# Kernel tuning notes

Hardware: AMD Instinct MI355X
Metric: run time of the kernel (lower is better)

Reference implementation:

```python
import jax, jax.numpy as jnp
import numpy as np

D_MODEL = 1024
NHEAD = 16
HEAD_DIM = D_MODEL // NHEAD
B, T = 2, 2048


def setup_inputs() -> dict:
    key = jax.random.key(0)
    ks = jax.random.split(key, 11)
    s = 1.0 / np.sqrt(D_MODEL)
    inp = {
        'q': jax.random.normal(ks[0], (B, T, D_MODEL), jnp.float32),
        'k': jax.random.normal(ks[1], (B, T, D_MODEL), jnp.float32),
        'v': jax.random.normal(ks[2], (B, T, D_MODEL), jnp.float32),
        'Wq': jax.random.normal(ks[3], (D_MODEL, D_MODEL), jnp.float32) * s,
        'bq': jnp.zeros((D_MODEL,), jnp.float32),
        'Wk': jax.random.normal(ks[4], (D_MODEL, D_MODEL), jnp.float32) * s,
        'bk': jnp.zeros((D_MODEL,), jnp.float32),
        'Wv': jax.random.normal(ks[5], (D_MODEL, D_MODEL), jnp.float32) * s,
        'bv': jnp.zeros((D_MODEL,), jnp.float32),
        'Wo': jax.random.normal(ks[6], (D_MODEL, D_MODEL), jnp.float32) * s,
        'bo': jnp.zeros((D_MODEL,), jnp.float32),
    }
    return inp


def reference(q, k, v, Wq, bq, Wk, bk, Wv, bv, Wo, bo):
    scale = np.sqrt(HEAD_DIM).astype(np.float32)
    # projections (torch Linear: x @ W.T + b), split heads -> [B, H, T, Dh]
    def proj(x, W, b):
        y = jnp.einsum('btd,ed->bte', x, W) + b
        return y.reshape(B, T, NHEAD, HEAD_DIM).transpose(0, 2, 1, 3)
    qh = proj(q, Wq, bq)
    kh = proj(k, Wk, bk)
    vh = proj(v, Wv, bv)
    scores = jnp.einsum('bhqd,bhkd->bhqk', qh, kh) / scale  # [B,H,T,T]
    weights = jax.nn.softmax(scores, axis=-1)
    out = jnp.einsum('bhqk,bhkd->bhqd', weights, vh)        # [B,H,T,Dh]
    out = out.transpose(0, 2, 1, 3).reshape(B, T, D_MODEL)
    return jnp.einsum('btd,ed->bte', out, Wo) + bo
```

## Files before the change

kernel.cpp:

```cpp
#include <hip/hip_runtime.h>
#include <cstdint>
#include <cstddef>


#define D_MODEL 1024
#define NHEAD   16
#define HDIM    64
#define BATCH   2
#define SEQ     2048
#define BT      (BATCH * SEQ)

typedef __bf16 bf16;
typedef __bf16 bf16x8 __attribute__((ext_vector_type(8)));
typedef __bf16 bf16x4 __attribute__((ext_vector_type(4)));
typedef float  floatx4 __attribute__((ext_vector_type(4)));
typedef short  short4v __attribute__((ext_vector_type(4)));

#define MFMA16(a, b, c) __builtin_amdgcn_mfma_f32_16x16x32_bf16((a), (b), (c), 0, 0, 0)

__device__ __forceinline__ floatx4 MFMA16B(bf16x4 a, bf16x4 b, floatx4 c) {
  return __builtin_amdgcn_mfma_f32_16x16x16bf16_1k(
      __builtin_bit_cast(short4v, a), __builtin_bit_cast(short4v, b), c, 0, 0, 0);
}

__device__ __forceinline__ void async_cp16(const bf16* g, bf16* l) {
  __builtin_amdgcn_global_load_lds(
      (__attribute__((address_space(1))) void*)(g),
      (__attribute__((address_space(3))) void*)(l), 16, 0, 0);
}

__global__ __launch_bounds__(256) void cvt7(
    const float* __restrict__ s0, const float* __restrict__ s1,
    const float* __restrict__ s2, const float* __restrict__ s3,
    const float* __restrict__ s4, const float* __restrict__ s5,
    const float* __restrict__ s6,
    bf16* __restrict__ d0, bf16* __restrict__ d1, bf16* __restrict__ d2,
    bf16* __restrict__ d3, bf16* __restrict__ d4, bf16* __restrict__ d5,
    bf16* __restrict__ d6)
{
  const float* src; bf16* dst; int n4;
  switch (blockIdx.y) {
    case 0:  src = s0; dst = d0; n4 = (BT * D_MODEL) / 4; break;
    case 1:  src = s1; dst = d1; n4 = (BT * D_MODEL) / 4; break;
    case 2:  src = s2; dst = d2; n4 = (BT * D_MODEL) / 4; break;
    case 3:  src = s3; dst = d3; n4 = (D_MODEL * D_MODEL) / 4; break;
    case 4:  src = s4; dst = d4; n4 = (D_MODEL * D_MODEL) / 4; break;
    case 5:  src = s5; dst = d5; n4 = (D_MODEL * D_MODEL) / 4; break;
    default: src = s6; dst = d6; n4 = (D_MODEL * D_MODEL) / 4; break;
  }
  int stride = gridDim.x * blockDim.x;
  for (int i = blockIdx.x * blockDim.x + threadIdx.x; i < n4; i += stride) {
    float4 f = ((const float4*)src)[i];
    bf16x4 h;
    h[0] = (bf16)f.x; h[1] = (bf16)f.y; h[2] = (bf16)f.z; h[3] = (bf16)f.w;
    ((bf16x4*)dst)[i] = h;
  }
}

__device__ __forceinline__ void gemm128_core(
    const bf16* __restrict__ A, const bf16* __restrict__ W,
    int m0, int n0, bf16* As, bf16* Bs, floatx4 acc[4][4])
{
  const int t = threadIdx.x;
  const int l = t & 63, w = t >> 6;
  const int quad = l >> 4, lr = l & 15;
  const int wm = (w >> 1) * 64, wn = (w & 1) * 64;

  floatx4 z = {0.f, 0.f, 0.f, 0.f};
#pragma unroll
  for (int i = 0; i < 4; i++)
#pragma unroll
    for (int j = 0; j < 4; j++) acc[i][j] = z;

  for (int kt = 0; kt < 1024; kt += 32) {
    __syncthreads();
#pragma unroll
    for (int i = 0; i < 2; i++) {
      int c = i * 256 + t;
      int row = c >> 2, ci = c & 3;
      async_cp16(A + (size_t)(m0 + row) * 1024 + kt + ci * 8,
                 As + (i * 256 + w * 64) * 8);
      async_cp16(W + (size_t)(n0 + row) * 1024 + kt + ci * 8,
                 Bs + (i * 256 + w * 64) * 8);
    }
    __syncthreads();

    bf16x8 af[4], bfr[4];
#pragma unroll
    for (int i = 0; i < 4; i++) {
      af[i]  = *(const bf16x8*)(As + (wm + i * 16 + lr) * 32 + quad * 8);
      bfr[i] = *(const bf16x8*)(Bs + (wn + i * 16 + lr) * 32 + quad * 8);
    }
#pragma unroll
    for (int i = 0; i < 4; i++)
#pragma unroll
      for (int j = 0; j < 4; j++)
        acc[i][j] = MFMA16(af[i], bfr[j], acc[i][j]);
  }
}

__global__ __launch_bounds__(256) void qkv_gemm(
    const bf16* __restrict__ qb, const bf16* __restrict__ kb, const bf16* __restrict__ vb,
    const bf16* __restrict__ wq, const bf16* __restrict__ wk, const bf16* __restrict__ wv,
    const float* __restrict__ biasq, const float* __restrict__ biask, const float* __restrict__ biasv,
    bf16* __restrict__ qh, bf16* __restrict__ kh, bf16* __restrict__ vt)
{
  __shared__ bf16 As[128 * 32];
  __shared__ bf16 Bs[128 * 32];
  const int zid = blockIdx.z;
  const bf16* A = (zid == 0) ? qb : ((zid == 1) ? kb : vb);
  const bf16* W = (zid == 0) ? wq : ((zid == 1) ? wk : wv);
  const float* bias = (zid == 0) ? biasq : ((zid == 1) ? biask : biasv);
  const int m0 = blockIdx.x * 128, n0 = blockIdx.y * 128;

  floatx4 acc[4][4];
  gemm128_core(A, W, m0, n0, As, Bs, acc);

  const int t = threadIdx.x, l = t & 63, w = t >> 6;
  const int quad = l >> 4, lr = l & 15;
  const int wm = (w >> 1) * 64, wn = (w & 1) * 64;

  if (zid < 2) {
    bf16* out = (zid == 0) ? qh : kh;
#pragma unroll
    for (int i = 0; i < 4; i++) {
      int mbase = m0 + wm + i * 16 + quad * 4;
      int b  = mbase >> 11;
      int tq = mbase & 2047;
#pragma unroll
      for (int j = 0; j < 4; j++) {
        int n = n0 + wn + j * 16 + lr;
        float bv = bias[n];
        int h = n >> 6, dh = n & 63;
        bf16* p = out + ((size_t)((b * NHEAD + h) * SEQ + tq)) * HDIM + dh;
#pragma unroll
        for (int r = 0; r < 4; r++)
          p[(size_t)r * HDIM] = (bf16)(acc[i][j][r] + bv);
      }
    }
  } else {
#pragma unroll
    for (int i = 0; i < 4; i++) {
      int mbase = m0 + wm + i * 16 + quad * 4;
      int b  = mbase >> 11;
      int tq = mbase & 2047;
#pragma unroll
      for (int j = 0; j < 4; j++) {
        int n = n0 + wn + j * 16 + lr;
        float bv = bias[n];
        int h = n >> 6, dh = n & 63;
        bf16x4 pk;
#pragma unroll
        for (int r = 0; r < 4; r++) pk[r] = (bf16)(acc[i][j][r] + bv);
        *(bf16x4*)(vt + ((size_t)((b * NHEAD + h) * HDIM + dh)) * SEQ + tq) = pk;
      }
    }
  }
}

__global__ __launch_bounds__(512, 4) void attn_fused(
    const bf16* __restrict__ qh, const bf16* __restrict__ kh,
    const bf16* __restrict__ vt, bf16* __restrict__ attn)
{
  __shared__ __align__(16) char smem[35840];
  bf16* Ks  = (bf16*)smem;
  bf16* Vts = (bf16*)(smem + 18432);
  bf16* Ost = (bf16*)smem;

  const int t = threadIdx.x, l = t & 63, w = t >> 6;
  const int quad = l >> 4, lr = l & 15;
  const int bh = blockIdx.y;
  const int qt0 = blockIdx.x * 128;
  const bf16* qg = qh + (size_t)bh * SEQ * HDIM;
  const bf16* kg = kh + (size_t)bh * SEQ * HDIM;
  const bf16* vg = vt + (size_t)bh * HDIM * SEQ;

  bf16x8 qf[2];
#pragma unroll
  for (int ko = 0; ko < 2; ko++)
    qf[ko] = *(const bf16x8*)(qg + (size_t)(qt0 + w * 16 + lr) * HDIM
                              + ko * 32 + quad * 8);

  floatx4 zz = {0.f, 0.f, 0.f, 0.f};
  floatx4 Oacc[4];
#pragma unroll
  for (int dt = 0; dt < 4; dt++) Oacc[dt] = zz;
  float mrow = -3.0e38f, lrow = 0.f;
  const float scale = 0.125f;

  for (int kt0 = 0; kt0 < SEQ; kt0 += 128) {
    __syncthreads();
#pragma unroll
    for (int i = 0; i < 2; i++) {
      int c = t + 512 * i;
      { int row = c >> 3, ci = c & 7;
        *(int4*)(Ks + row * 72 + ci * 8) =
            *(const int4*)(kg + (size_t)(kt0 + row) * HDIM + ci * 8); }
      { int row = c >> 4, ci = c & 15;
        *(int4*)(Vts + row * 136 + ci * 8) =
            *(const int4*)(vg + (size_t)row * SEQ + kt0 + ci * 8); }
    }
    __syncthreads();

    floatx4 s[8];
#pragma unroll
    for (int ni = 0; ni < 8; ni++) {
      const bf16* krow = Ks + (ni * 16 + lr) * 72 + quad * 8;
      bf16x8 k0 = *(const bf16x8*)(krow);
      bf16x8 k1 = *(const bf16x8*)(krow + 32);
      floatx4 a = zz;
      a = MFMA16(k0, qf[0], a);
      a = MFMA16(k1, qf[1], a);
      s[ni] = a;
    }

    float rmax = s[0][0];
#pragma unroll
    for (int ni = 0; ni < 8; ni++)
#pragma unroll
      for (int r = 0; r < 4; r++) rmax = fmaxf(rmax, s[ni][r]);
    rmax = fmaxf(rmax, __shfl_xor(rmax, 16, 64));
    rmax = fmaxf(rmax, __shfl_xor(rmax, 32, 64));
    float mnew = fmaxf(mrow, rmax * scale);
    float al = __expf(mrow - mnew);
    mrow = mnew;

    bf16x4 pk[8];
    float rsum = 0.f;
#pragma unroll
    for (int ni = 0; ni < 8; ni++)
#pragma unroll
      for (int r = 0; r < 4; r++) {
        float pv = __expf(s[ni][r] * scale - mnew);
        rsum += pv;
        pk[ni][r] = (bf16)pv;
      }
    rsum += __shfl_xor(rsum, 16, 64);
    rsum += __shfl_xor(rsum, 32, 64);
    lrow = lrow * al + rsum;
#pragma unroll
    for (int dt = 0; dt < 4; dt++)
#pragma unroll
      for (int r = 0; r < 4; r++) Oacc[dt][r] *= al;

#pragma unroll
    for (int ni = 0; ni < 8; ni++)
#pragma unroll
      for (int dt = 0; dt < 4; dt++) {
        bf16x4 vf = *(const bf16x4*)(Vts + (dt * 16 + lr) * 136
                                     + ni * 16 + quad * 4);
        Oacc[dt] = MFMA16B(vf, pk[ni], Oacc[dt]);
      }
  }

  float inv = 1.0f / lrow;
  __syncthreads();
#pragma unroll
  for (int dt = 0; dt < 4; dt++) {
    bf16x4 ov;
#pragma unroll
    for (int r = 0; r < 4; r++) ov[r] = (bf16)(Oacc[dt][r] * inv);
    *(bf16x4*)(Ost + (size_t)(w * 16 + lr) * 72 + dt * 16 + quad * 4) = ov;
  }
  __syncthreads();

  const int b = bh >> 4, h = bh & 15;
#pragma unroll
  for (int i = 0; i < 2; i++) {
    int c = t + 512 * i;
    int row = c >> 3, ci = c & 7;
    *(int4*)(attn + ((size_t)b * SEQ + qt0 + row) * D_MODEL + h * HDIM + ci * 8) =
        *(const int4*)(Ost + row * 72 + ci * 8);
  }
}

__global__ __launch_bounds__(256) void oproj_gemm(
    const bf16* __restrict__ attn, const bf16* __restrict__ wo,
    const float* __restrict__ bo, float* __restrict__ out)
{
  __shared__ bf16 As[128 * 32];
  __shared__ bf16 Bs[128 * 32];
  const int m0 = blockIdx.x * 128, n0 = blockIdx.y * 128;

  floatx4 acc[4][4];
  gemm128_core(attn, wo, m0, n0, As, Bs, acc);

  const int t = threadIdx.x, l = t & 63, w = t >> 6;
  const int quad = l >> 4, lr = l & 15;
  const int wm = (w >> 1) * 64, wn = (w & 1) * 64;

#pragma unroll
  for (int i = 0; i < 4; i++) {
    int m = m0 + wm + i * 16 + quad * 4;
#pragma unroll
    for (int j = 0; j < 4; j++) {
      int n = n0 + wn + j * 16 + lr;
      float bv = bo[n];
      float* p = out + (size_t)m * D_MODEL + n;
#pragma unroll
      for (int r = 0; r < 4; r++)
        p[(size_t)r * D_MODEL] = acc[i][j][r] + bv;
    }
  }
}

extern "C" void kernel_launch(void* const* d_in, const int* in_sizes, int n_in,
                              void* d_out, int out_size, void* d_ws, size_t ws_size,
                              hipStream_t stream)
{
  const float* q  = (const float*)d_in[0];
  const float* k  = (const float*)d_in[1];
  const float* v  = (const float*)d_in[2];
  const float* Wq = (const float*)d_in[3];
  const float* bq = (const float*)d_in[4];
  const float* Wk = (const float*)d_in[5];
  const float* bk = (const float*)d_in[6];
  const float* Wv = (const float*)d_in[7];
  const float* bv = (const float*)d_in[8];
  const float* Wo = (const float*)d_in[9];
  const float* bo = (const float*)d_in[10];

  const size_t NQ = (size_t)BT * D_MODEL;
  const size_t NW = (size_t)D_MODEL * D_MODEL;

  bf16* p = (bf16*)d_ws;
  bf16* qb   = p; p += NQ;
  bf16* kb   = p; p += NQ;
  bf16* vb   = p; p += NQ;
  bf16* wqb  = p; p += NW;
  bf16* wkb  = p; p += NW;
  bf16* wvb  = p; p += NW;
  bf16* wob  = p; p += NW;
  bf16* qhp  = p; p += NQ;
  bf16* khp  = p; p += NQ;
  bf16* vtp  = p; p += NQ;
  bf16* attn = p; p += NQ;

  cvt7<<<dim3(1024, 7, 1), 256, 0, stream>>>(q, k, v, Wq, Wk, Wv, Wo,
                                             qb, kb, vb, wqb, wkb, wvb, wob);
  qkv_gemm<<<dim3(32, 8, 3), 256, 0, stream>>>(qb, kb, vb, wqb, wkb, wvb,
                                               bq, bk, bv, qhp, khp, vtp);
  attn_fused<<<dim3(16, 32, 1), 512, 0, stream>>>(qhp, khp, vtp, attn);
  oproj_gemm<<<dim3(32, 8, 1), 256, 0, stream>>>(attn, wob, bo, (float*)d_out);
}
```

Measured before the change: 238.6 us.

## Split attention keys across wave halves, fold scale into Q, shrink oproj tiles

Folds the softmax scale and log2(e) into the Q projection so the attention softmax can use exp2 directly. The attention kernel now handles 64 query rows per block, with two wave groups each covering half of every key tile. Their partial softmax states are merged through shared memory at the end. The grid is doubled and launch bounds raised to 6 to get more parallelism and occupancy. The output projection uses 64x64 tiles with async global-to-LDS loads to launch more blocks, at the cost of less data reuse per block and a more complex merge step.

```diff
diff --git a/kernel.cpp b/kernel.cpp
--- a/kernel.cpp
+++ b/kernel.cpp
@@ -10,6 +10,8 @@
 #define SEQ     2048
 #define BT      (BATCH * SEQ)
 
+#define QSCALE 0.18033688011112043f
+
 typedef __bf16 bf16;
 typedef __bf16 bf16x8 __attribute__((ext_vector_type(8)));
 typedef __bf16 bf16x4 __attribute__((ext_vector_type(4)));
@@ -21,6 +23,10 @@
 __device__ __forceinline__ floatx4 MFMA16B(bf16x4 a, bf16x4 b, floatx4 c) {
   return __builtin_amdgcn_mfma_f32_16x16x16bf16_1k(
       __builtin_bit_cast(short4v, a), __builtin_bit_cast(short4v, b), c, 0, 0, 0);
+}
+
+__device__ __forceinline__ float fexp2(float x) {
+  return __builtin_amdgcn_exp2f(x);
 }
 
 __device__ __forceinline__ void async_cp16(const bf16* g, bf16* l) {
@@ -119,6 +125,7 @@
   const int t = threadIdx.x, l = t & 63, w = t >> 6;
   const int quad = l >> 4, lr = l & 15;
   const int wm = (w >> 1) * 64, wn = (w & 1) * 64;
+  const float sc = (zid == 0) ? QSCALE : 1.0f;
 
   if (zid < 2) {
     bf16* out = (zid == 0) ? qh : kh;
@@ -135,7 +142,7 @@
         bf16* p = out + ((size_t)((b * NHEAD + h) * SEQ + tq)) * HDIM + dh;
 #pragma unroll
         for (int r = 0; r < 4; r++)
-          p[(size_t)r * HDIM] = (bf16)(acc[i][j][r] + bv);
+          p[(size_t)r * HDIM] = (bf16)((acc[i][j][r] + bv) * sc);
       }
     }
   } else {
@@ -158,27 +165,27 @@
   }
 }
 
-__global__ __launch_bounds__(512, 4) void attn_fused(
+__global__ __launch_bounds__(512, 6) void attn_fused(
     const bf16* __restrict__ qh, const bf16* __restrict__ kh,
     const bf16* __restrict__ vt, bf16* __restrict__ attn)
 {
   __shared__ __align__(16) char smem[35840];
   bf16* Ks  = (bf16*)smem;
   bf16* Vts = (bf16*)(smem + 18432);
-  bf16* Ost = (bf16*)smem;
 
   const int t = threadIdx.x, l = t & 63, w = t >> 6;
   const int quad = l >> 4, lr = l & 15;
+  const int qg = w & 3, half = w >> 2;
   const int bh = blockIdx.y;
-  const int qt0 = blockIdx.x * 128;
-  const bf16* qg = qh + (size_t)bh * SEQ * HDIM;
-  const bf16* kg = kh + (size_t)bh * SEQ * HDIM;
-  const bf16* vg = vt + (size_t)bh * HDIM * SEQ;
+  const int qt0 = blockIdx.x * 64;
+  const bf16* qg_ = qh + (size_t)bh * SEQ * HDIM;
+  const bf16* kg  = kh + (size_t)bh * SEQ * HDIM;
+  const bf16* vg  = vt + (size_t)bh * HDIM * SEQ;
 
   bf16x8 qf[2];
 #pragma unroll
   for (int ko = 0; ko < 2; ko++)
-    qf[ko] = *(const bf16x8*)(qg + (size_t)(qt0 + w * 16 + lr) * HDIM
+    qf[ko] = *(const bf16x8*)(qg_ + (size_t)(qt0 + qg * 16 + lr) * HDIM
                               + ko * 32 + quad * 8);
 
   floatx4 zz = {0.f, 0.f, 0.f, 0.f};
@@ -186,7 +193,6 @@
 #pragma unroll
   for (int dt = 0; dt < 4; dt++) Oacc[dt] = zz;
   float mrow = -3.0e38f, lrow = 0.f;
-  const float scale = 0.125f;
 
   for (int kt0 = 0; kt0 < SEQ; kt0 += 128) {
     __syncthreads();
@@ -202,10 +208,10 @@
     }
     __syncthreads();
 
-    floatx4 s[8];
-#pragma unroll
-    for (int ni = 0; ni < 8; ni++) {
-      const bf16* krow = Ks + (ni * 16 + lr) * 72 + quad * 8;
+    floatx4 s[4];
+#pragma unroll
+    for (int ni = 0; ni < 4; ni++) {
+      const bf16* krow = Ks + (half * 64 + ni * 16 + lr) * 72 + quad * 8;
       bf16x8 k0 = *(const bf16x8*)(krow);
       bf16x8 k1 = *(const bf16x8*)(krow + 32);
       floatx4 a = zz;
@@ -216,22 +222,22 @@
 
     float rmax = s[0][0];
 #pragma unroll
-    for (int ni = 0; ni < 8; ni++)
+    for (int ni = 0; ni < 4; ni++)
 #pragma unroll
       for (int r = 0; r < 4; r++) rmax = fmaxf(rmax, s[ni][r]);
     rmax = fmaxf(rmax, __shfl_xor(rmax, 16, 64));
     rmax = fmaxf(rmax, __shfl_xor(rmax, 32, 64));
-    float mnew = fmaxf(mrow, rmax * scale);
-    float al = __expf(mrow - mnew);
+    float mnew = fmaxf(mrow, rmax);
+    float al = fexp2(mrow - mnew);
     mrow = mnew;
 
-    bf16x4 pk[8];
+    bf16x4 pk[4];
     float rsum = 0.f;
 #pragma unroll
-    for (int ni = 0; ni < 8; ni++)
+    for (int ni = 0; ni < 4; ni++)
 #pragma unroll
       for (int r = 0; r < 4; r++) {
-        float pv = __expf(s[ni][r] * scale - mnew);
+        float pv = fexp2(s[ni][r] - mnew);
         rsum += pv;
         pk[ni][r] = (bf16)pv;
       }
@@ -244,31 +250,49 @@
       for (int r = 0; r < 4; r++) Oacc[dt][r] *= al;
 
 #pragma unroll
-    for (int ni = 0; ni < 8; ni++)
+    for (int ni = 0; ni < 4; ni++)
 #pragma unroll
       for (int dt = 0; dt < 4; dt++) {
         bf16x4 vf = *(const bf16x4*)(Vts + (dt * 16 + lr) * 136
-                                     + ni * 16 + quad * 4);
+                                     + half * 64 + ni * 16 + quad * 4);
         Oacc[dt] = MFMA16B(vf, pk[ni], Oacc[dt]);
       }
   }
 
-  float inv = 1.0f / lrow;
   __syncthreads();
-#pragma unroll
-  for (int dt = 0; dt < 4; dt++) {
-    bf16x4 ov;
-#pragma unroll
-    for (int r = 0; r < 4; r++) ov[r] = (bf16)(Oacc[dt][r] * inv);
-    *(bf16x4*)(Ost + (size_t)(w * 16 + lr) * 72 + dt * 16 + quad * 4) = ov;
+  bf16* Ost = (bf16*)(smem + 16896);
+
+  if (half == 1) {
+#pragma unroll
+    for (int dt = 0; dt < 4; dt++)
+      *(floatx4*)(smem + (qg * 4 + dt) * 1024 + l * 16) = Oacc[dt];
+    if (quad == 0)
+      *(float2*)(smem + 16384 + (qg * 16 + lr) * 8) = make_float2(mrow, lrow);
   }
   __syncthreads();
 
+  if (half == 0) {
+    float2 st = *(const float2*)(smem + 16384 + (qg * 16 + lr) * 8);
+    float ms = fmaxf(mrow, st.x);
+    float fA = fexp2(mrow - ms);
+    float fB = fexp2(st.x - ms);
+    float inv = 1.0f / (lrow * fA + st.y * fB);
+    float gA = fA * inv, gB = fB * inv;
+#pragma unroll
+    for (int dt = 0; dt < 4; dt++) {
+      floatx4 ob = *(const floatx4*)(smem + (qg * 4 + dt) * 1024 + l * 16);
+      bf16x4 ov;
+#pragma unroll
+      for (int r = 0; r < 4; r++)
+        ov[r] = (bf16)(Oacc[dt][r] * gA + ob[r] * gB);
+      *(bf16x4*)(Ost + (size_t)(qg * 16 + lr) * 72 + dt * 16 + quad * 4) = ov;
+    }
+  }
+  __syncthreads();
+
   const int b = bh >> 4, h = bh & 15;
-#pragma unroll
-  for (int i = 0; i < 2; i++) {
-    int c = t + 512 * i;
-    int row = c >> 3, ci = c & 7;
+  {
+    int row = t >> 3, ci = t & 7;
     *(int4*)(attn + ((size_t)b * SEQ + qt0 + row) * D_MODEL + h * HDIM + ci * 8) =
         *(const int4*)(Ost + row * 72 + ci * 8);
   }
@@ -278,22 +302,49 @@
     const bf16* __restrict__ attn, const bf16* __restrict__ wo,
     const float* __restrict__ bo, float* __restrict__ out)
 {
-  __shared__ bf16 As[128 * 32];
-  __shared__ bf16 Bs[128 * 32];
-  const int m0 = blockIdx.x * 128, n0 = blockIdx.y * 128;
-
-  floatx4 acc[4][4];
-  gemm128_core(attn, wo, m0, n0, As, Bs, acc);
-
+  __shared__ bf16 As[64 * 32];
+  __shared__ bf16 Bs[64 * 32];
+  const int m0 = blockIdx.x * 64, n0 = blockIdx.y * 64;
   const int t = threadIdx.x, l = t & 63, w = t >> 6;
   const int quad = l >> 4, lr = l & 15;
-  const int wm = (w >> 1) * 64, wn = (w & 1) * 64;
-
-#pragma unroll
-  for (int i = 0; i < 4; i++) {
+  const int wm = (w >> 1) * 32, wn = (w & 1) * 32;
+
+  floatx4 z = {0.f, 0.f, 0.f, 0.f};
+  floatx4 acc[2][2];
+#pragma unroll
+  for (int i = 0; i < 2; i++)
+#pragma unroll
+    for (int j = 0; j < 2; j++) acc[i][j] = z;
+
+  for (int kt = 0; kt < 1024; kt += 32) {
+    __syncthreads();
+    {
+      int row = t >> 2, ci = t & 3;
+      async_cp16(attn + (size_t)(m0 + row) * 1024 + kt + ci * 8,
+                 As + (w * 64) * 8);
+      async_cp16(wo + (size_t)(n0 + row) * 1024 + kt + ci * 8,
+                 Bs + (w * 64) * 8);
+    }
+    __syncthreads();
+
+    bf16x8 af[2], bfr[2];
+#pragma unroll
+    for (int i = 0; i < 2; i++) {
+      af[i]  = *(const bf16x8*)(As + (wm + i * 16 + lr) * 32 + quad * 8);
+      bfr[i] = *(const bf16x8*)(Bs + (wn + i * 16 + lr) * 32 + quad * 8);
+    }
+#pragma unroll
+    for (int i = 0; i < 2; i++)
+#pragma unroll
+      for (int j = 0; j < 2; j++)
+        acc[i][j] = MFMA16(af[i], bfr[j], acc[i][j]);
+  }
+
+#pragma unroll
+  for (int i = 0; i < 2; i++) {
     int m = m0 + wm + i * 16 + quad * 4;
 #pragma unroll
-    for (int j = 0; j < 4; j++) {
+    for (int j = 0; j < 2; j++) {
       int n = n0 + wn + j * 16 + lr;
       float bv = bo[n];
       float* p = out + (size_t)m * D_MODEL + n;
@@ -340,6 +391,6 @@
                                              qb, kb, vb, wqb, wkb, wvb, wob);
   qkv_gemm<<<dim3(32, 8, 3), 256, 0, stream>>>(qb, kb, vb, wqb, wkb, wvb,
                                                bq, bk, bv, qhp, khp, vtp);
-  attn_fused<<<dim3(16, 32, 1), 512, 0, stream>>>(qhp, khp, vtp, attn);
-  oproj_gemm<<<dim3(32, 8, 1), 256, 0, stream>>>(attn, wob, bo, (float*)d_out);
-}
+  attn_fused<<<dim3(32, 32, 1), 512, 0, stream>>>(qhp, khp, vtp, attn);
+  oproj_gemm<<<dim3(64, 16, 1), 256, 0, stream>>>(attn, wob, bo, (float*)d_out);
+}
```

Result: slower. 258.4 us (+8.3%).
